# Optimization experiments

Hardware: AMD Instinct MI355X
Metric: run time of the kernel (lower is better)

The kernel has to match this reference:

```python
import jax, jax.numpy as jnp
import numpy as np

N_EMBD = 1024
HEAD_SIZE = 128
B, T = 8, 2048


def apply_rope(x):
    # x: (B, T, D); rotate interleaved pairs, matching torch view(B,T,D//2,2)
    b, t, d = x.shape
    freqs = 1.0 / (10000.0 ** (jnp.arange(0, d, 2, dtype=jnp.float32) / d))  # (D//2,)
    angles = jnp.arange(t, dtype=jnp.float32)[:, None] * freqs[None, :]      # (T, D//2)
    cos_a = jnp.cos(angles).astype(x.dtype)
    sin_a = jnp.sin(angles).astype(x.dtype)
    xr = x.reshape(b, t, d // 2, 2)
    x0, x1 = xr[..., 0], xr[..., 1]
    rot = jnp.stack([x0 * cos_a - x1 * sin_a, x0 * sin_a + x1 * cos_a], axis=-1)
    return rot.reshape(b, t, d)


def setup_inputs() -> dict:
    key = jax.random.key(0)
    kx, kq, kk, kv = jax.random.split(key, 4)
    x = jax.random.normal(kx, (B, T, N_EMBD), dtype=jnp.float32)
    scale = 0.02
    Wq = jax.random.normal(kq, (N_EMBD, HEAD_SIZE), dtype=jnp.float32) * scale
    Wk = jax.random.normal(kk, (N_EMBD, HEAD_SIZE), dtype=jnp.float32) * scale
    Wv = jax.random.normal(kv, (N_EMBD, HEAD_SIZE), dtype=jnp.float32) * scale
    return {"x": x, "Wq": Wq, "Wk": Wk, "Wv": Wv}


def reference(x, Wq, Wk, Wv):
    # QKV projections (bias=False)
    q = x @ Wq  # (B, T, H)
    k = x @ Wk
    v = x @ Wv
    q = apply_rope(q)
    k = apply_rope(k)
    d = k.shape[-1]
    wei = jnp.einsum('bqd,bkd->bqk', q, k) * (d ** -0.5)  # (B, T, T)
    causal = jnp.tril(jnp.ones((q.shape[1], q.shape[1]), dtype=bool))
    wei = jnp.where(causal, wei, jnp.finfo(wei.dtype).min)
    wei = jax.nn.softmax(wei, axis=-1)
    out = jnp.einsum('bqk,bkd->bqd', wei, v)  # (B, T, H)
    return out
```

## Files before the change

### kernel.cpp

```cpp
#include <hip/hip_runtime.h>
#include <math.h>

#define BB 8
#define TT 2048
#define EE 1024
#define DD 128

typedef _Float16 f16x8 __attribute__((ext_vector_type(8)));
typedef _Float16 f16x4 __attribute__((ext_vector_type(4)));
typedef float    f32x4 __attribute__((ext_vector_type(4)));
typedef float    f32x16 __attribute__((ext_vector_type(16)));

#define QSCALE 0.12752406f


__global__ __launch_bounds__(256)
void wt_prep_kernel(const float* __restrict__ Wq,
                    const float* __restrict__ Wk,
                    const float* __restrict__ Wv,
                    _Float16* __restrict__ Wb)
{
    int gid = blockIdx.x * 256 + threadIdx.x;
    int kc  = gid / 768;
    int rem = gid - kc * 768;
    int ns  = rem >> 6;
    int ln  = rem & 63;
    int n   = ns * 32 + (ln & 31);
    int k0  = kc * 16 + (ln >> 5) * 8;
    const float* __restrict__ W = (n < 128) ? Wq : (n < 256) ? Wk : Wv;
    int nl = n & 127;
    f16x8 w;
#pragma unroll
    for (int j = 0; j < 8; j++)
        w[j] = (_Float16)W[(size_t)(k0 + j) * DD + nl];
    *(f16x8*)&Wb[(size_t)gid * 8] = w;
}

__global__ __launch_bounds__(512)
void proj_rope_kernel(const float* __restrict__ x,
                      const _Float16* __restrict__ Wb,
                      _Float16* __restrict__ Qb,
                      _Float16* __restrict__ Ka,
                      _Float16* __restrict__ Va)
{
    const int r0   = blockIdx.x * 64;
    const int tid  = threadIdx.x;
    const int wave = tid >> 6;
    const int lane = tid & 63;
    const int half = lane >> 5;
    const int col  = lane & 31;
    const int wave_m = wave & 1;
    const int wave_n = wave >> 1;

    __shared__ _Float16 Xb[2][4096];
    __shared__ _Float16 Out[64][136];

    f32x16 acc[3];
#pragma unroll
    for (int s = 0; s < 3; s++) acc[s] = (f32x16)0.f;

    const int sr = tid >> 3;
    const int sc = (tid & 7) * 4;
    const float* __restrict__ xp = &x[(size_t)(r0 + sr) * EE + sc];
    const int sm = sr >> 5, rr = sr & 31;
    const int w0 = (((sc      >> 4) * 2 + sm) << 9) + ((rr + 32 * ((sc       >> 3) & 1)) << 3) + (sc & 7);
    const int w1 = ((((sc+32) >> 4) * 2 + sm) << 9) + ((rr + 32 * (((sc+32)  >> 3) & 1)) << 3) + (sc & 7);

    float4 pa0 = *(const float4*)(xp);
    float4 pa1 = *(const float4*)(xp + 32);
    {
        f16x4 h0 = { (_Float16)pa0.x, (_Float16)pa0.y, (_Float16)pa0.z, (_Float16)pa0.w };
        f16x4 h1 = { (_Float16)pa1.x, (_Float16)pa1.y, (_Float16)pa1.z, (_Float16)pa1.w };
        *(f16x4*)&Xb[0][w0] = h0;
        *(f16x4*)&Xb[0][w1] = h1;
    }
    float4 na0 = *(const float4*)(xp + 64);
    float4 na1 = *(const float4*)(xp + 96);

    for (int it = 0; it < 16; it++) {
        const int buf = it & 1;
        __syncthreads();
#pragma unroll
        for (int kc = 0; kc < 4; kc++) {
            f16x8 a = *(f16x8*)&Xb[buf][((kc * 2 + wave_m) << 9) + lane * 8];
#pragma unroll
            for (int s = 0; s < 3; s++) {
                f16x8 b = *(const f16x8*)&Wb[((size_t)(it * 4 + kc) * 12 + wave_n * 3 + s) * 512 + lane * 8];
                acc[s] = __builtin_amdgcn_mfma_f32_32x32x16_f16(a, b, acc[s], 0, 0, 0);
            }
        }
        if (it + 1 < 16) {
            f16x4 h0 = { (_Float16)na0.x, (_Float16)na0.y, (_Float16)na0.z, (_Float16)na0.w };
            f16x4 h1 = { (_Float16)na1.x, (_Float16)na1.y, (_Float16)na1.z, (_Float16)na1.w };
            *(f16x4*)&Xb[buf ^ 1][w0] = h0;
            *(f16x4*)&Xb[buf ^ 1][w1] = h1;
        }
        if (it + 2 < 16) {
            na0 = *(const float4*)(xp + (it + 2) * 64);
            na1 = *(const float4*)(xp + (it + 2) * 64 + 32);
        }
    }

    const int bidx = r0 >> 11;
    const int t0   = r0 & (TT - 1);

    for (int p = 0; p < 3; p++) {
        __syncthreads();
#pragma unroll
        for (int s = 0; s < 3; s++) {
            int gs = wave_n * 3 + s;
            if ((gs >> 2) != p) continue;
            int dcol = (gs & 3) * 32 + col;
            float f = 0.f;
            if (p < 2)
                f = __powf(10000.0f, -(float)(dcol & ~1) * (1.0f / 128.0f));
#pragma unroll
            for (int rg = 0; rg < 16; rg++) {
                int mrow = wave_m * 32 + (rg & 3) + 8 * (rg >> 2) + 4 * half;
                float av = acc[s][rg];
                float res;
                if (p < 2) {
                    float ap = __shfl_xor(av, 1);
                    float sa, ca;
                    __sincosf((float)(t0 + mrow) * f, &sa, &ca);
                    res = av * ca + ap * ((dcol & 1) ? sa : -sa);
                    if (p == 0) res *= QSCALE;
                } else {
                    res = av;
                }
                Out[mrow][dcol] = (_Float16)res;
            }
        }
        __syncthreads();
        if (p < 2) {
            _Float16* __restrict__ dst = (p == 0) ? Qb : Ka;
#pragma unroll
            for (int jj = 0; jj < 2; jj++) {
                int cid = tid + 512 * jj;
                int sl = cid >> 9, kc = (cid >> 6) & 7, ln = cid & 63;
                f16x8 v8 = *(f16x8*)&Out[sl * 32 + (ln & 31)][kc * 16 + (ln >> 5) * 8];
                size_t ga = ((((size_t)bidx * 64 + (t0 >> 5) + sl) * 8 + kc) * 64 + ln) * 8;
                *(f16x8*)&dst[ga] = v8;
            }
        } else {
#pragma unroll
            for (int jj = 0; jj < 2; jj++) {
                int cid = tid + 512 * jj;
                int kcl = cid >> 8, ds = (cid >> 6) & 3, ln = cid & 63;
                f16x8 vv;
#pragma unroll
                for (int e = 0; e < 8; e++)
                    vv[e] = Out[kcl * 16 + (ln >> 5) * 8 + e][ds * 32 + (ln & 31)];
                size_t ga = ((((size_t)bidx * 128 + (t0 >> 4) + kcl) * 4 + ds) * 64 + ln) * 8;
                *(f16x8*)&Va[ga] = vv;
            }
        }
    }
}

__global__ __launch_bounds__(256)
void attn_kernel(const _Float16* __restrict__ Qb,
                 const _Float16* __restrict__ Ka,
                 const _Float16* __restrict__ Va,
                 _Float16* __restrict__ opart,
                 float* __restrict__ mpart,
                 float* __restrict__ lpart)
{
    const int b  = blockIdx.y;
    const int v_ = 39 - blockIdx.x;
    int xt, c;
    if (v_ < 4)       { xt = v_;                  c = 0; }
    else if (v_ < 12) { xt = 4 + ((v_ - 4) >> 1); c = (v_ - 4) & 1; }
    else if (v_ < 24) { xt = 8 + (v_ - 12) / 3;   c = (v_ - 12) % 3; }
    else              { xt = 12 + ((v_ - 24) >> 2); c = (v_ - 24) & 3; }
    const int q0 = xt * 128;
    const int nt = 2 * xt + 2;
    const int kt_begin = c * 8;
    const int kt_end   = (kt_begin + 8 < nt) ? (kt_begin + 8) : nt;

    const int tid  = threadIdx.x;
    const int wave = tid >> 6;
    const int lane = tid & 63;
    const int half = lane >> 5;
    const int col  = lane & 31;

    __shared__ _Float16 Kb[8192];
    __shared__ _Float16 Vb[8192];
    __shared__ _Float16 Ps[4][32][72];

    const _Float16* __restrict__ kst = Ka + (size_t)b * 64 * 4096;
    const _Float16* __restrict__ vst = Va + (size_t)b * 128 * 2048;

    const int qg = q0 + wave * 32 + col;
    f16x8 qb[8];
#pragma unroll
    for (int kc = 0; kc < 8; kc++)
        qb[kc] = *(const f16x8*)&Qb[((((size_t)b * 64 + xt * 4 + wave) * 8 + kc) * 64 + lane) * 8];

    f32x16 Of[4];
#pragma unroll
    for (int t = 0; t < 4; t++) Of[t] = (f32x16)0.f;
    float m_ = -1e30f, l_ = 0.f;

    f16x8 kr[4], vr[4];
    {
        const _Float16* kp = kst + (size_t)kt_begin * 8192;
        const _Float16* vp = vst + (size_t)kt_begin * 8192;
#pragma unroll
        for (int i = 0; i < 4; i++) kr[i] = *(const f16x8*)&kp[(tid + 256 * i) * 8];
#pragma unroll
        for (int i = 0; i < 4; i++) vr[i] = *(const f16x8*)&vp[(tid + 256 * i) * 8];
    }

    for (int kt = kt_begin; kt < kt_end; kt++) {
        const int kb0 = kt * 64;
        __syncthreads();
#pragma unroll
        for (int i = 0; i < 4; i++) *(f16x8*)&Kb[(tid + 256 * i) * 8] = kr[i];
#pragma unroll
        for (int i = 0; i < 4; i++) *(f16x8*)&Vb[(tid + 256 * i) * 8] = vr[i];
        __syncthreads();
        if (kt + 1 < kt_end) {
            const _Float16* kp = kst + (size_t)(kt + 1) * 8192;
            const _Float16* vp = vst + (size_t)(kt + 1) * 8192;
#pragma unroll
            for (int i = 0; i < 4; i++) kr[i] = *(const f16x8*)&kp[(tid + 256 * i) * 8];
#pragma unroll
            for (int i = 0; i < 4; i++) vr[i] = *(const f16x8*)&vp[(tid + 256 * i) * 8];
        }

        f32x16 sf[2];
#pragma unroll
        for (int g = 0; g < 2; g++) {
            sf[g] = (f32x16)0.f;
#pragma unroll
            for (int kc = 0; kc < 8; kc++) {
                f16x8 kf = *(f16x8*)&Kb[((g * 8 + kc) * 64 + lane) * 8];
                sf[g] = __builtin_amdgcn_mfma_f32_32x32x16_f16(kf, qb[kc], sf[g], 0, 0, 0);
            }
        }

        const bool diag = (kt >= 2 * xt);
        float mloc = -1e30f;
#pragma unroll
        for (int g = 0; g < 2; g++)
#pragma unroll
            for (int rg = 0; rg < 16; rg++) {
                int key = kb0 + g * 32 + (rg & 3) + 8 * (rg >> 2) + 4 * half;
                float val = sf[g][rg];
                val = (!diag || key <= qg) ? val : -1e30f;
                sf[g][rg] = val;
                mloc = fmaxf(mloc, val);
            }
        mloc = fmaxf(mloc, __shfl_xor(mloc, 32));
        float mnew  = fmaxf(m_, mloc);
        float alpha = __builtin_amdgcn_exp2f(m_ - mnew);
        float ps = 0.f;
#pragma unroll
        for (int g = 0; g < 2; g++) {
#pragma unroll
            for (int rc = 0; rc < 4; rc++) {
                f16x4 p4;
#pragma unroll
                for (int rr = 0; rr < 4; rr++) {
                    float p = __builtin_amdgcn_exp2f(sf[g][4 * rc + rr] - mnew);
                    ps += p;
                    p4[rr] = (_Float16)p;
                }
                *(f16x4*)&Ps[wave][col][g * 32 + 8 * rc + 4 * half] = p4;
            }
        }
        ps += __shfl_xor(ps, 32);
        l_ = l_ * alpha + ps;
        m_ = mnew;
#pragma unroll
        for (int t = 0; t < 4; t++) Of[t] *= alpha;

        f16x8 pb[4];
#pragma unroll
        for (int kc = 0; kc < 4; kc++)
            pb[kc] = *(f16x8*)&Ps[wave][col][kc * 16 + half * 8];
#pragma unroll
        for (int t = 0; t < 4; t++) {
#pragma unroll
            for (int kcl = 0; kcl < 4; kcl++) {
                f16x8 vf = *(f16x8*)&Vb[((kcl * 4 + t) * 64 + lane) * 8];
                Of[t] = __builtin_amdgcn_mfma_f32_32x32x16_f16(vf, pb[kcl], Of[t], 0, 0, 0);
            }
        }
    }

    const int slot = (b * 16 + xt) * 4 + c;
    _Float16* op = opart + ((size_t)slot * 128 + wave * 32 + col) * DD;
#pragma unroll
    for (int t = 0; t < 4; t++) {
#pragma unroll
        for (int rc = 0; rc < 4; rc++) {
            f16x4 o4 = { (_Float16)Of[t][4 * rc + 0], (_Float16)Of[t][4 * rc + 1],
                         (_Float16)Of[t][4 * rc + 2], (_Float16)Of[t][4 * rc + 3] };
            *(f16x4*)&op[t * 32 + 8 * rc + 4 * half] = o4;
        }
    }
    if (half == 0) {
        mpart[slot * 128 + wave * 32 + col] = m_;
        lpart[slot * 128 + wave * 32 + col] = l_;
    }
}

__global__ __launch_bounds__(256)
void combine_kernel(const _Float16* __restrict__ opart,
                    const float* __restrict__ mpart,
                    const float* __restrict__ lpart,
                    float* __restrict__ out)
{
    int gid = blockIdx.x * 256 + threadIdx.x;
    int d   = gid & 127;
    int t   = gid >> 7;
    int b   = t >> 11;
    int tl  = t & (TT - 1);
    int xt  = tl >> 7;
    int rl  = tl & 127;
    int np  = (2 * xt + 2 + 7) >> 3;
    int sb  = (b * 16 + xt) * 4;

    float mm = -1e30f;
    for (int j = 0; j < np; j++)
        mm = fmaxf(mm, mpart[(sb + j) * 128 + rl]);
    float acc = 0.f, den = 0.f;
    for (int j = 0; j < np; j++) {
        float w = __builtin_amdgcn_exp2f(mpart[(sb + j) * 128 + rl] - mm);
        den += w * lpart[(sb + j) * 128 + rl];
        acc += w * (float)opart[((size_t)(sb + j) * 128 + rl) * DD + d];
    }
    out[gid] = acc / den;
}

extern "C" void kernel_launch(void* const* d_in, const int* in_sizes, int n_in,
                              void* d_out, int out_size, void* d_ws, size_t ws_size,
                              hipStream_t stream)
{
    const float* x  = (const float*)d_in[0];
    const float* Wq = (const float*)d_in[1];
    const float* Wk = (const float*)d_in[2];
    const float* Wv = (const float*)d_in[3];
    float* out = (float*)d_out;

    const size_t NTOK = (size_t)BB * TT;
    _Float16* Qb = (_Float16*)d_ws;
    _Float16* Ka = Qb + NTOK * DD;
    _Float16* Va = Ka + NTOK * DD;
    _Float16* Wb = Va + NTOK * DD;
    _Float16* opart = Wb + (size_t)384 * EE;
    float* mp = (float*)(opart + (size_t)512 * 128 * DD);
    float* lp = mp + 512 * 128;

    wt_prep_kernel<<<dim3(192), dim3(256), 0, stream>>>(Wq, Wk, Wv, Wb);
    proj_rope_kernel<<<dim3(256), dim3(512), 0, stream>>>(x, Wb, Qb, Ka, Va);
    attn_kernel<<<dim3(40, BB), dim3(256), 0, stream>>>(Qb, Ka, Va, opart, mp, lp);
    combine_kernel<<<dim3((int)(NTOK * DD / 256)), dim3(256), 0, stream>>>(opart, mp, lp, out);
}
```

Before: 168.0 us.

## Halve projection tile rows and split attention KV range into finer chunks

The projection kernel now processes 32 rows per block with 4 waves, doubling the block count to 512. Its loop hoists all A/B fragment loads ahead of the MFMAs and prefetches x one more iteration ahead. The attention split-KV chunk shrinks from 8 to 4 key tiles, raising the grid from 40 to 72 blocks per batch to fill more CUs, with combine and workspace sizes adjusted to match. The cost is more partial outputs to write and merge in the combine step, and less reuse of each weight fragment in the projection.

Result: no change. 170.5 us (+1.5%).

```diff
diff --git a/kernel.cpp b/kernel.cpp
--- a/kernel.cpp
+++ b/kernel.cpp
@@ -36,24 +36,22 @@
     *(f16x8*)&Wb[(size_t)gid * 8] = w;
 }
 
-__global__ __launch_bounds__(512)
+__global__ __launch_bounds__(256)
 void proj_rope_kernel(const float* __restrict__ x,
                       const _Float16* __restrict__ Wb,
                       _Float16* __restrict__ Qb,
                       _Float16* __restrict__ Ka,
                       _Float16* __restrict__ Va)
 {
-    const int r0   = blockIdx.x * 64;
+    const int r0   = blockIdx.x * 32;
     const int tid  = threadIdx.x;
     const int wave = tid >> 6;
     const int lane = tid & 63;
     const int half = lane >> 5;
     const int col  = lane & 31;
-    const int wave_m = wave & 1;
-    const int wave_n = wave >> 1;
-
-    __shared__ _Float16 Xb[2][4096];
-    __shared__ _Float16 Out[64][136];
+
+    __shared__ _Float16 Xb[2][2048];
+    __shared__ _Float16 Out[32][136];
 
     f32x16 acc[3];
 #pragma unroll
@@ -62,9 +60,8 @@
     const int sr = tid >> 3;
     const int sc = (tid & 7) * 4;
     const float* __restrict__ xp = &x[(size_t)(r0 + sr) * EE + sc];
-    const int sm = sr >> 5, rr = sr & 31;
-    const int w0 = (((sc      >> 4) * 2 + sm) << 9) + ((rr + 32 * ((sc       >> 3) & 1)) << 3) + (sc & 7);
-    const int w1 = ((((sc+32) >> 4) * 2 + sm) << 9) + ((rr + 32 * (((sc+32)  >> 3) & 1)) << 3) + (sc & 7);
+    const int w0 = ((sc        >> 4) << 9) + ((sr + 32 * ((sc        >> 3) & 1)) << 3) + (sc & 7);
+    const int w1 = (((sc + 32) >> 4) << 9) + ((sr + 32 * (((sc + 32) >> 3) & 1)) << 3) + (sc & 7);
 
     float4 pa0 = *(const float4*)(xp);
     float4 pa1 = *(const float4*)(xp + 32);
@@ -76,28 +73,36 @@
     }
     float4 na0 = *(const float4*)(xp + 64);
     float4 na1 = *(const float4*)(xp + 96);
+    float4 nb0 = *(const float4*)(xp + 128);
+    float4 nb1 = *(const float4*)(xp + 160);
 
     for (int it = 0; it < 16; it++) {
         const int buf = it & 1;
         __syncthreads();
-#pragma unroll
-        for (int kc = 0; kc < 4; kc++) {
-            f16x8 a = *(f16x8*)&Xb[buf][((kc * 2 + wave_m) << 9) + lane * 8];
-#pragma unroll
-            for (int s = 0; s < 3; s++) {
-                f16x8 b = *(const f16x8*)&Wb[((size_t)(it * 4 + kc) * 12 + wave_n * 3 + s) * 512 + lane * 8];
-                acc[s] = __builtin_amdgcn_mfma_f32_32x32x16_f16(a, b, acc[s], 0, 0, 0);
-            }
-        }
+        f16x8 a[4], b[12];
+#pragma unroll
+        for (int kc = 0; kc < 4; kc++)
+            a[kc] = *(f16x8*)&Xb[buf][(kc << 9) + lane * 8];
+#pragma unroll
+        for (int kc = 0; kc < 4; kc++)
+#pragma unroll
+            for (int s = 0; s < 3; s++)
+                b[kc * 3 + s] = *(const f16x8*)&Wb[((size_t)(it * 4 + kc) * 12 + wave * 3 + s) * 512 + lane * 8];
+#pragma unroll
+        for (int kc = 0; kc < 4; kc++)
+#pragma unroll
+            for (int s = 0; s < 3; s++)
+                acc[s] = __builtin_amdgcn_mfma_f32_32x32x16_f16(a[kc], b[kc * 3 + s], acc[s], 0, 0, 0);
         if (it + 1 < 16) {
             f16x4 h0 = { (_Float16)na0.x, (_Float16)na0.y, (_Float16)na0.z, (_Float16)na0.w };
             f16x4 h1 = { (_Float16)na1.x, (_Float16)na1.y, (_Float16)na1.z, (_Float16)na1.w };
             *(f16x4*)&Xb[buf ^ 1][w0] = h0;
             *(f16x4*)&Xb[buf ^ 1][w1] = h1;
-        }
-        if (it + 2 < 16) {
-            na0 = *(const float4*)(xp + (it + 2) * 64);
-            na1 = *(const float4*)(xp + (it + 2) * 64 + 32);
+            na0 = nb0; na1 = nb1;
+        }
+        if (it + 3 < 16) {
+            nb0 = *(const float4*)(xp + (it + 3) * 64);
+            nb1 = *(const float4*)(xp + (it + 3) * 64 + 32);
         }
     }
 
@@ -108,7 +113,7 @@
         __syncthreads();
 #pragma unroll
         for (int s = 0; s < 3; s++) {
-            int gs = wave_n * 3 + s;
+            int gs = wave * 3 + s;
             if ((gs >> 2) != p) continue;
             int dcol = (gs & 3) * 32 + col;
             float f = 0.f;
@@ -116,7 +121,7 @@
                 f = __powf(10000.0f, -(float)(dcol & ~1) * (1.0f / 128.0f));
 #pragma unroll
             for (int rg = 0; rg < 16; rg++) {
-                int mrow = wave_m * 32 + (rg & 3) + 8 * (rg >> 2) + 4 * half;
+                int mrow = (rg & 3) + 8 * (rg >> 2) + 4 * half;
                 float av = acc[s][rg];
                 float res;
                 if (p < 2) {
@@ -136,16 +141,16 @@
             _Float16* __restrict__ dst = (p == 0) ? Qb : Ka;
 #pragma unroll
             for (int jj = 0; jj < 2; jj++) {
-                int cid = tid + 512 * jj;
-                int sl = cid >> 9, kc = (cid >> 6) & 7, ln = cid & 63;
-                f16x8 v8 = *(f16x8*)&Out[sl * 32 + (ln & 31)][kc * 16 + (ln >> 5) * 8];
-                size_t ga = ((((size_t)bidx * 64 + (t0 >> 5) + sl) * 8 + kc) * 64 + ln) * 8;
+                int cid = tid + 256 * jj;
+                int kc = cid >> 6, ln = cid & 63;
+                f16x8 v8 = *(f16x8*)&Out[ln & 31][kc * 16 + (ln >> 5) * 8];
+                size_t ga = ((((size_t)bidx * 64 + (t0 >> 5)) * 8 + kc) * 64 + ln) * 8;
                 *(f16x8*)&dst[ga] = v8;
             }
         } else {
 #pragma unroll
             for (int jj = 0; jj < 2; jj++) {
-                int cid = tid + 512 * jj;
+                int cid = tid + 256 * jj;
                 int kcl = cid >> 8, ds = (cid >> 6) & 3, ln = cid & 63;
                 f16x8 vv;
 #pragma unroll
@@ -166,17 +171,20 @@
                  float* __restrict__ mpart,
                  float* __restrict__ lpart)
 {
-    const int b  = blockIdx.y;
-    const int v_ = 39 - blockIdx.x;
-    int xt, c;
-    if (v_ < 4)       { xt = v_;                  c = 0; }
-    else if (v_ < 12) { xt = 4 + ((v_ - 4) >> 1); c = (v_ - 4) & 1; }
-    else if (v_ < 24) { xt = 8 + (v_ - 12) / 3;   c = (v_ - 12) % 3; }
-    else              { xt = 12 + ((v_ - 24) >> 2); c = (v_ - 24) & 3; }
+    const int b = blockIdx.y;
+    int xt = 15, c = 0;
+    {
+        int v = 71 - blockIdx.x, s0 = 0;
+        for (int j = 0; j < 16; j++) {
+            int nc = (j + 2) >> 1;
+            if (v < s0 + nc) { xt = j; c = v - s0; break; }
+            s0 += nc;
+        }
+    }
     const int q0 = xt * 128;
     const int nt = 2 * xt + 2;
-    const int kt_begin = c * 8;
-    const int kt_end   = (kt_begin + 8 < nt) ? (kt_begin + 8) : nt;
+    const int kt_begin = c * 4;
+    const int kt_end   = (kt_begin + 4 < nt) ? (kt_begin + 4) : nt;
 
     const int tid  = threadIdx.x;
     const int wave = tid >> 6;
@@ -290,7 +298,7 @@
         }
     }
 
-    const int slot = (b * 16 + xt) * 4 + c;
+    const int slot = (b * 16 + xt) * 8 + c;
     _Float16* op = opart + ((size_t)slot * 128 + wave * 32 + col) * DD;
 #pragma unroll
     for (int t = 0; t < 4; t++) {
@@ -320,8 +328,8 @@
     int tl  = t & (TT - 1);
     int xt  = tl >> 7;
     int rl  = tl & 127;
-    int np  = (2 * xt + 2 + 7) >> 3;
-    int sb  = (b * 16 + xt) * 4;
+    int np  = (2 * xt + 5) >> 2;
+    int sb  = (b * 16 + xt) * 8;
 
     float mm = -1e30f;
     for (int j = 0; j < np; j++)
@@ -351,11 +359,11 @@
     _Float16* Va = Ka + NTOK * DD;
     _Float16* Wb = Va + NTOK * DD;
     _Float16* opart = Wb + (size_t)384 * EE;
-    float* mp = (float*)(opart + (size_t)512 * 128 * DD);
-    float* lp = mp + 512 * 128;
+    float* mp = (float*)(opart + (size_t)1024 * 128 * DD);
+    float* lp = mp + 1024 * 128;
 
     wt_prep_kernel<<<dim3(192), dim3(256), 0, stream>>>(Wq, Wk, Wv, Wb);
-    proj_rope_kernel<<<dim3(256), dim3(512), 0, stream>>>(x, Wb, Qb, Ka, Va);
-    attn_kernel<<<dim3(40, BB), dim3(256), 0, stream>>>(Qb, Ka, Va, opart, mp, lp);
+    proj_rope_kernel<<<dim3(512), dim3(256), 0, stream>>>(x, Wb, Qb, Ka, Va);
+    attn_kernel<<<dim3(72, BB), dim3(256), 0, stream>>>(Qb, Ka, Va, opart, mp, lp);
     combine_kernel<<<dim3((int)(NTOK * DD / 256)), dim3(256), 0, stream>>>(opart, mp, lp, out);
 }
```

## Load x directly into MFMA registers in projection, drop LDS staging, halve row tile

Applied to the files above, without the earlier changes.

The projection kernel now uses 32-row tiles with 256 threads and twice as many blocks. Each lane loads its fp32 x fragment from global memory straight into registers and converts it to fp16 for the MFMA A operand. This removes the LDS double buffer and its per-iteration barriers. All weight fragments for an iteration are prefetched into registers, and the launch bound asks for two blocks per CU. The cost is that four waves now read the same x rows redundantly, and the gathered global loads are less coalesced.

Result: slower. 188.7 us (+12.3%).

```diff
diff --git a/kernel.cpp b/kernel.cpp
--- a/kernel.cpp
+++ b/kernel.cpp
@@ -36,68 +36,53 @@
     *(f16x8*)&Wb[(size_t)gid * 8] = w;
 }
 
-__global__ __launch_bounds__(512)
+__global__ __launch_bounds__(256, 2)
 void proj_rope_kernel(const float* __restrict__ x,
                       const _Float16* __restrict__ Wb,
                       _Float16* __restrict__ Qb,
                       _Float16* __restrict__ Ka,
                       _Float16* __restrict__ Va)
 {
-    const int r0   = blockIdx.x * 64;
+    const int r0   = blockIdx.x * 32;
     const int tid  = threadIdx.x;
     const int wave = tid >> 6;
     const int lane = tid & 63;
     const int half = lane >> 5;
     const int col  = lane & 31;
-    const int wave_m = wave & 1;
-    const int wave_n = wave >> 1;
-
-    __shared__ _Float16 Xb[2][4096];
-    __shared__ _Float16 Out[64][136];
+
+    __shared__ _Float16 Out[32][136];
 
     f32x16 acc[3];
 #pragma unroll
     for (int s = 0; s < 3; s++) acc[s] = (f32x16)0.f;
 
-    const int sr = tid >> 3;
-    const int sc = (tid & 7) * 4;
-    const float* __restrict__ xp = &x[(size_t)(r0 + sr) * EE + sc];
-    const int sm = sr >> 5, rr = sr & 31;
-    const int w0 = (((sc      >> 4) * 2 + sm) << 9) + ((rr + 32 * ((sc       >> 3) & 1)) << 3) + (sc & 7);
-    const int w1 = ((((sc+32) >> 4) * 2 + sm) << 9) + ((rr + 32 * (((sc+32)  >> 3) & 1)) << 3) + (sc & 7);
-
-    float4 pa0 = *(const float4*)(xp);
-    float4 pa1 = *(const float4*)(xp + 32);
-    {
-        f16x4 h0 = { (_Float16)pa0.x, (_Float16)pa0.y, (_Float16)pa0.z, (_Float16)pa0.w };
-        f16x4 h1 = { (_Float16)pa1.x, (_Float16)pa1.y, (_Float16)pa1.z, (_Float16)pa1.w };
-        *(f16x4*)&Xb[0][w0] = h0;
-        *(f16x4*)&Xb[0][w1] = h1;
-    }
-    float4 na0 = *(const float4*)(xp + 64);
-    float4 na1 = *(const float4*)(xp + 96);
+    const float* __restrict__ xrow = &x[(size_t)(r0 + col) * EE + half * 8];
 
     for (int it = 0; it < 16; it++) {
-        const int buf = it & 1;
-        __syncthreads();
+        f32x4 xa[4][2];
+        f16x8 b[12];
 #pragma unroll
         for (int kc = 0; kc < 4; kc++) {
-            f16x8 a = *(f16x8*)&Xb[buf][((kc * 2 + wave_m) << 9) + lane * 8];
-#pragma unroll
-            for (int s = 0; s < 3; s++) {
-                f16x8 b = *(const f16x8*)&Wb[((size_t)(it * 4 + kc) * 12 + wave_n * 3 + s) * 512 + lane * 8];
-                acc[s] = __builtin_amdgcn_mfma_f32_32x32x16_f16(a, b, acc[s], 0, 0, 0);
-            }
-        }
-        if (it + 1 < 16) {
-            f16x4 h0 = { (_Float16)na0.x, (_Float16)na0.y, (_Float16)na0.z, (_Float16)na0.w };
-            f16x4 h1 = { (_Float16)na1.x, (_Float16)na1.y, (_Float16)na1.z, (_Float16)na1.w };
-            *(f16x4*)&Xb[buf ^ 1][w0] = h0;
-            *(f16x4*)&Xb[buf ^ 1][w1] = h1;
-        }
-        if (it + 2 < 16) {
-            na0 = *(const float4*)(xp + (it + 2) * 64);
-            na1 = *(const float4*)(xp + (it + 2) * 64 + 32);
+            const float* p = xrow + it * 64 + kc * 16;
+            xa[kc][0] = *(const f32x4*)(p);
+            xa[kc][1] = *(const f32x4*)(p + 4);
+        }
+#pragma unroll
+        for (int kc = 0; kc < 4; kc++)
+#pragma unroll
+            for (int s = 0; s < 3; s++)
+                b[kc * 3 + s] = *(const f16x8*)&Wb[((size_t)(it * 4 + kc) * 12 + wave * 3 + s) * 512 + lane * 8];
+#pragma unroll
+        for (int kc = 0; kc < 4; kc++) {
+            f16x8 a;
+#pragma unroll
+            for (int j = 0; j < 4; j++) {
+                a[j]     = (_Float16)xa[kc][0][j];
+                a[j + 4] = (_Float16)xa[kc][1][j];
+            }
+#pragma unroll
+            for (int s = 0; s < 3; s++)
+                acc[s] = __builtin_amdgcn_mfma_f32_32x32x16_f16(a, b[kc * 3 + s], acc[s], 0, 0, 0);
         }
     }
 
@@ -108,7 +93,7 @@
         __syncthreads();
 #pragma unroll
         for (int s = 0; s < 3; s++) {
-            int gs = wave_n * 3 + s;
+            int gs = wave * 3 + s;
             if ((gs >> 2) != p) continue;
             int dcol = (gs & 3) * 32 + col;
             float f = 0.f;
@@ -116,7 +101,7 @@
                 f = __powf(10000.0f, -(float)(dcol & ~1) * (1.0f / 128.0f));
 #pragma unroll
             for (int rg = 0; rg < 16; rg++) {
-                int mrow = wave_m * 32 + (rg & 3) + 8 * (rg >> 2) + 4 * half;
+                int mrow = (rg & 3) + 8 * (rg >> 2) + 4 * half;
                 float av = acc[s][rg];
                 float res;
                 if (p < 2) {
@@ -136,16 +121,16 @@
             _Float16* __restrict__ dst = (p == 0) ? Qb : Ka;
 #pragma unroll
             for (int jj = 0; jj < 2; jj++) {
-                int cid = tid + 512 * jj;
-                int sl = cid >> 9, kc = (cid >> 6) & 7, ln = cid & 63;
-                f16x8 v8 = *(f16x8*)&Out[sl * 32 + (ln & 31)][kc * 16 + (ln >> 5) * 8];
-                size_t ga = ((((size_t)bidx * 64 + (t0 >> 5) + sl) * 8 + kc) * 64 + ln) * 8;
+                int cid = tid + 256 * jj;
+                int kc = cid >> 6, ln = cid & 63;
+                f16x8 v8 = *(f16x8*)&Out[ln & 31][kc * 16 + (ln >> 5) * 8];
+                size_t ga = ((((size_t)bidx * 64 + (t0 >> 5)) * 8 + kc) * 64 + ln) * 8;
                 *(f16x8*)&dst[ga] = v8;
             }
         } else {
 #pragma unroll
             for (int jj = 0; jj < 2; jj++) {
-                int cid = tid + 512 * jj;
+                int cid = tid + 256 * jj;
                 int kcl = cid >> 8, ds = (cid >> 6) & 3, ln = cid & 63;
                 f16x8 vv;
 #pragma unroll
@@ -355,7 +340,7 @@
     float* lp = mp + 512 * 128;
 
     wt_prep_kernel<<<dim3(192), dim3(256), 0, stream>>>(Wq, Wk, Wv, Wb);
-    proj_rope_kernel<<<dim3(256), dim3(512), 0, stream>>>(x, Wb, Qb, Ka, Va);
+    proj_rope_kernel<<<dim3(512), dim3(256), 0, stream>>>(x, Wb, Qb, Ka, Va);
     attn_kernel<<<dim3(40, BB), dim3(256), 0, stream>>>(Qb, Ka, Va, opart, mp, lp);
     combine_kernel<<<dim3((int)(NTOK * DD / 256)), dim3(256), 0, stream>>>(opart, mp, lp, out);
 }
```
